# Kernel optimization log

Measured on AMD Instinct MI355X. Metric: run time of the kernel, lower is better.

The kernel has to match this reference:

```python
import jax, jax.numpy as jnp
import numpy as np

DIM = 384
HEADS = 6
HIDDEN = int(DIM * 4.0)
EPS = 1e-6

def setup_inputs() -> dict:
    key = jax.random.key(0)
    ks = jax.random.split(key, 8)
    s = 0.02
    return {
        "x": jax.random.normal(ks[0], (4, 2048, DIM), dtype=jnp.float32),
        "w_qkv": jax.random.normal(ks[1], (DIM, 3 * DIM), dtype=jnp.float32) * s,
        "b_qkv": jnp.zeros((3 * DIM,), dtype=jnp.float32),
        "w_proj": jax.random.normal(ks[2], (DIM, DIM), dtype=jnp.float32) * s,
        "b_proj": jnp.zeros((DIM,), dtype=jnp.float32),
        "w_fc1": jax.random.normal(ks[3], (DIM, HIDDEN), dtype=jnp.float32) * s,
        "b_fc1": jnp.zeros((HIDDEN,), dtype=jnp.float32),
        "w_fc2": jax.random.normal(ks[4], (HIDDEN, DIM), dtype=jnp.float32) * s,
        "b_fc2": jnp.zeros((DIM,), dtype=jnp.float32),
        "g1": jnp.ones((DIM,), dtype=jnp.float32),
        "beta1": jnp.zeros((DIM,), dtype=jnp.float32),
        "g2": jnp.ones((DIM,), dtype=jnp.float32),
        "beta2": jnp.zeros((DIM,), dtype=jnp.float32),
    }

def _layernorm(x, g, b):
    mu = jnp.mean(x, axis=-1, keepdims=True)
    var = jnp.mean(jnp.square(x - mu), axis=-1, keepdims=True)
    return (x - mu) * jax.lax.rsqrt(var + EPS) * g + b

def _attention(x, w_qkv, b_qkv, w_proj, b_proj):
    B, N, C = x.shape
    H = HEADS
    Dh = C // H
    qkv = x @ w_qkv + b_qkv                      # [B,N,3C]
    qkv = qkv.reshape(B, N, 3, H, Dh)
    q = jnp.transpose(qkv[:, :, 0], (0, 2, 1, 3))  # [B,H,N,Dh]
    k = jnp.transpose(qkv[:, :, 1], (0, 2, 1, 3))
    v = jnp.transpose(qkv[:, :, 2], (0, 2, 1, 3))
    scale = Dh ** -0.5
    attn = jnp.einsum('bhnd,bhmd->bhnm', q, k) * scale
    attn = jax.nn.softmax(attn, axis=-1)
    out = jnp.einsum('bhnm,bhmd->bhnd', attn, v)
    out = jnp.transpose(out, (0, 2, 1, 3)).reshape(B, N, C)
    return out @ w_proj + b_proj

def _mlp(x, w_fc1, b_fc1, w_fc2, b_fc2):
    h = jax.nn.gelu(x @ w_fc1 + b_fc1, approximate=False)
    return h @ w_fc2 + b_fc2

def reference(x, w_qkv, b_qkv, w_proj, b_proj, w_fc1, b_fc1, w_fc2, b_fc2, g1, beta1, g2, beta2):
    x = x + _attention(_layernorm(x, g1, beta1), w_qkv, b_qkv, w_proj, b_proj)
    x = x + _mlp(_layernorm(x, g2, beta2), w_fc1, b_fc1, w_fc2, b_fc2)
    return x
```

## Files before the change

### kernel.cpp

```cpp
#include <hip/hip_runtime.h>
#include <hip/hip_bf16.h>

#define TOK 8192
#define CDIM 384
#define HEADS 6
#define DH 64
#define HID 1536
#define SEQ 2048

#define QSCALE 0.18033688011112042f

typedef short bf16x8 __attribute__((ext_vector_type(8)));
typedef short bf16x4 __attribute__((ext_vector_type(4)));
typedef float f32x4 __attribute__((ext_vector_type(4)));
typedef float f32x16 __attribute__((ext_vector_type(16)));
typedef void __attribute__((address_space(1))) GV;
typedef void __attribute__((address_space(3))) SV;

__device__ __forceinline__ short f2bf(float f) {
    __hip_bfloat16 h = __float2bfloat16(f);
    return *reinterpret_cast<short*>(&h);
}

__device__ __forceinline__ int pack_bf2(float a, float b) {
    __hip_bfloat162 h2 = __float22bfloat162_rn(make_float2(a, b));
    int r;
    __builtin_memcpy(&r, &h2, 4);
    return r;
}

__device__ __forceinline__ void gl_lds16(const short* g, short* lds) {
    __builtin_amdgcn_global_load_lds((GV*)g, (SV*)lds, 16, 0, 0);
}

__device__ __forceinline__ float gelu_fast(float v) {
    const float A = 2.3022067f;
    const float B = 0.1029442f;
    const float u = v * (A + B * v * v);
    return v - v / (1.0f + exp2f(u));
}

__global__ __launch_bounds__(128) void ln_trans(const float* __restrict__ x,
                                                const float* __restrict__ g,
                                                const float* __restrict__ bta,
                                                short* __restrict__ y,
                                                const float* __restrict__ w_qkv,
                                                const float* __restrict__ w_proj,
                                                const float* __restrict__ w_fc1,
                                                const float* __restrict__ w_fc2,
                                                short* __restrict__ qkvT,
                                                short* __restrict__ projT,
                                                short* __restrict__ fc1T,
                                                short* __restrict__ fc2T) {
    if (blockIdx.x < TOK) {
        const int row = blockIdx.x;
        const float* xr = x + (size_t)row * CDIM;
        const int t = threadIdx.x;
        float v0 = xr[t], v1 = xr[t + 128], v2 = xr[t + 256];
        float s = v0 + v1 + v2;
        float ss = v0 * v0 + v1 * v1 + v2 * v2;
#pragma unroll
        for (int off = 1; off < 64; off <<= 1) {
            s += __shfl_xor(s, off);
            ss += __shfl_xor(ss, off);
        }
        __shared__ float sh[4];
        const int wv = t >> 6;
        if ((t & 63) == 0) { sh[wv] = s; sh[2 + wv] = ss; }
        __syncthreads();
        s = sh[0] + sh[1];
        ss = sh[2] + sh[3];
        const float mu = s * (1.0f / CDIM);
        const float var = ss * (1.0f / CDIM) - mu * mu;
        const float rs = rsqrtf(var + 1e-6f);
        short* yr = y + (size_t)row * CDIM;
        yr[t]       = f2bf((v0 - mu) * rs * g[t]       + bta[t]);
        yr[t + 128] = f2bf((v1 - mu) * rs * g[t + 128] + bta[t + 128]);
        yr[t + 256] = f2bf((v2 - mu) * rs * g[t + 256] + bta[t + 256]);
        return;
    }
    int b = blockIdx.x - TOK;
    const float* w; short* o; int K, N, nb;
    if (b < 432)       { w = w_qkv;  o = qkvT;  K = 384;  N = 1152; nb = 36; }
    else if (b < 576)  { b -= 432;  w = w_proj; o = projT; K = 384;  N = 384;  nb = 12; }
    else if (b < 1152) { b -= 576;  w = w_fc1;  o = fc1T;  K = 384;  N = 1536; nb = 48; }
    else               { b -= 1152; w = w_fc2;  o = fc2T;  K = 1536; N = 384;  nb = 12; }
    const int bx = (b % nb) * 32, by = (b / nb) * 32;
    __shared__ float t[32][33];
    const int tx = threadIdx.x & 31, ty = threadIdx.x >> 5;
#pragma unroll
    for (int i = 0; i < 8; ++i)
        t[ty + i * 4][tx] = w[(size_t)(by + ty + i * 4) * N + bx + tx];
    __syncthreads();
#pragma unroll
    for (int i = 0; i < 8; ++i)
        o[(size_t)(bx + ty + i * 4) * K + by + tx] = f2bf(t[tx][ty + i * 4]);
}

__global__ __launch_bounds__(128) void ln_kernel(const float* __restrict__ x,
                                                 const float* __restrict__ g,
                                                 const float* __restrict__ bta,
                                                 short* __restrict__ y) {
    const int row = blockIdx.x;
    const float* xr = x + (size_t)row * CDIM;
    const int t = threadIdx.x;
    float v0 = xr[t], v1 = xr[t + 128], v2 = xr[t + 256];
    float s = v0 + v1 + v2;
    float ss = v0 * v0 + v1 * v1 + v2 * v2;
#pragma unroll
    for (int off = 1; off < 64; off <<= 1) {
        s += __shfl_xor(s, off);
        ss += __shfl_xor(ss, off);
    }
    __shared__ float sh[4];
    const int wv = t >> 6;
    if ((t & 63) == 0) { sh[wv] = s; sh[2 + wv] = ss; }
    __syncthreads();
    s = sh[0] + sh[1];
    ss = sh[2] + sh[3];
    const float mu = s * (1.0f / CDIM);
    const float var = ss * (1.0f / CDIM) - mu * mu;
    const float rs = rsqrtf(var + 1e-6f);
    short* yr = y + (size_t)row * CDIM;
    yr[t]       = f2bf((v0 - mu) * rs * g[t]       + bta[t]);
    yr[t + 128] = f2bf((v1 - mu) * rs * g[t + 128] + bta[t + 128]);
    yr[t + 256] = f2bf((v2 - mu) * rs * g[t + 256] + bta[t + 256]);
}

template <int MODE, int MT>
__global__ __launch_bounds__(256) void mfma_gemm(const short* __restrict__ A,
                                                 const short* __restrict__ WT,
                                                 const float* __restrict__ bias,
                                                 const float* __restrict__ resid,
                                                 float* __restrict__ outF,
                                                 short* __restrict__ outB,
                                                 short* __restrict__ qb,
                                                 short* __restrict__ kb,
                                                 short* __restrict__ vtb,
                                                 int M, int N, int K) {
    constexpr int BN = (MT == 4) ? 128 : 64;
    constexpr int BM = (MT == 1) ? 64 : 128;
    __shared__ __align__(16) short As[BM * 64];
    __shared__ __align__(16) short Bs[BN * 64];

    const int tid  = threadIdx.x;
    const int w    = tid >> 6;
    const int lane = tid & 63;
    const int quad = lane >> 4;
    const int n15  = lane & 15;
    const int wr   = (MT == 4) ? (w >> 1) : w;
    const int wc   = (MT == 4) ? (w & 1) : 0;
    const int m0   = blockIdx.y * BM;
    const int n0   = blockIdx.x * BN;
    const int swz  = n15 & 7;

    f32x4 acc[MT][4];
#pragma unroll
    for (int i = 0; i < MT; ++i)
#pragma unroll
        for (int j = 0; j < 4; ++j) {
            acc[i][j][0] = 0; acc[i][j][1] = 0; acc[i][j][2] = 0; acc[i][j][3] = 0;
        }

    for (int k0 = 0; k0 < K; k0 += 64) {
        __syncthreads();
#pragma unroll
        for (int i = 0; i < BM / 32; ++i) {
            const int c = i * 256 + tid;
            const int r = c >> 3, p = c & 7;
            gl_lds16(A + (size_t)(m0 + r) * K + k0 + ((p ^ (r & 7)) * 8),
                     As + (i * 256 + w * 64) * 8);
        }
#pragma unroll
        for (int i = 0; i < BN / 32; ++i) {
            const int c = i * 256 + tid;
            const int r = c >> 3, p = c & 7;
            gl_lds16(WT + (size_t)(n0 + r) * K + k0 + ((p ^ (r & 7)) * 8),
                     Bs + (i * 256 + w * 64) * 8);
        }
        __syncthreads();

#pragma unroll
        for (int kk = 0; kk < 2; ++kk) {
            bf16x8 af[MT], bfr[4];
#pragma unroll
            for (int mt = 0; mt < MT; ++mt)
                af[mt] = *(const bf16x8*)&As[(wr * (MT * 16) + mt * 16 + n15) * 64 +
                                             (((kk * 4 + quad) ^ swz) * 8)];
#pragma unroll
            for (int nt = 0; nt < 4; ++nt)
                bfr[nt] = *(const bf16x8*)&Bs[(wc * 64 + nt * 16 + n15) * 64 +
                                              (((kk * 4 + quad) ^ swz) * 8)];
#pragma unroll
            for (int mt = 0; mt < MT; ++mt)
#pragma unroll
                for (int nt = 0; nt < 4; ++nt)
                    acc[mt][nt] = __builtin_amdgcn_mfma_f32_16x16x32_bf16(af[mt], bfr[nt], acc[mt][nt], 0, 0, 0);
        }
    }

#pragma unroll
    for (int nt = 0; nt < 4; ++nt) {
        const int col = n0 + wc * 64 + nt * 16 + n15;
        const float bv = bias[col];
        if constexpr (MODE == 2) {
            const int part = col / CDIM;
            const int rem  = col - part * CDIM;
            const int h    = rem >> 6;
            const int d    = rem & 63;
#pragma unroll
            for (int mt = 0; mt < MT; ++mt) {
                const int r0 = m0 + wr * (MT * 16) + mt * 16 + quad * 4;
                const int bi = r0 >> 11;
                const int n  = r0 & 2047;
                if (part == 2) {
                    short4 pkv;
                    pkv.x = f2bf(acc[mt][nt][0] + bv);
                    pkv.y = f2bf(acc[mt][nt][1] + bv);
                    pkv.z = f2bf(acc[mt][nt][2] + bv);
                    pkv.w = f2bf(acc[mt][nt][3] + bv);
                    *(short4*)&vtb[((size_t)(bi * HEADS + h) * DH + d) * SEQ + n] = pkv;
                } else {
                    short* dst = (part == 0 ? qb : kb) +
                                 ((size_t)(bi * HEADS + h) * SEQ + n) * DH + d;
#pragma unroll
                    for (int rr = 0; rr < 4; ++rr) {
                        float o = acc[mt][nt][rr] + bv;
                        if (part == 0) o *= QSCALE;
                        dst[(size_t)rr * DH] = f2bf(o);
                    }
                }
            }
        } else {
#pragma unroll
            for (int mt = 0; mt < MT; ++mt)
#pragma unroll
                for (int rr = 0; rr < 4; ++rr) {
                    const int r = m0 + wr * (MT * 16) + mt * 16 + quad * 4 + rr;
                    float o = acc[mt][nt][rr] + bv;
                    if constexpr (MODE == 1) {
                        outB[(size_t)r * N + col] = f2bf(gelu_fast(o));
                    } else {
                        if (resid) o += resid[(size_t)r * N + col];
                        outF[(size_t)r * N + col] = o;
                    }
                }
        }
    }
}

__global__ __launch_bounds__(256, 4) void attn_mfma(const short* __restrict__ qb,
                                                    const short* __restrict__ kb,
                                                    const short* __restrict__ vtb,
                                                    short* __restrict__ outp) {
    __shared__ __align__(16) char smem[33792];

    const int bid = blockIdx.x;
    const int x   = bid & 7;
    const int j   = bid >> 3;
    const int bh  = x * 3 + (j >> 6);
    const int qt  = j & 63;
    const int bi  = bh / HEADS;
    const int h   = bh - bi * HEADS;

    const int tid  = threadIdx.x;
    const int w    = tid >> 6;
    const int lane = tid & 63;
    const int l31  = lane & 31;
    const int hi   = lane >> 5;

    short* Kl  = (short*)(smem + w * 8192);
    short* Vtl = (short*)(smem + w * 8192 + 4096);

    const size_t headoff = (size_t)bh * SEQ * DH;

    bf16x8 qf[4];
    {
        const short* qg = qb + headoff + (size_t)(qt * 32 + l31) * DH + hi * 8;
#pragma unroll
        for (int kc = 0; kc < 4; ++kc)
            qf[kc] = *(const bf16x8*)(qg + kc * 16);
    }

    const int l3 = lane >> 3, l7 = lane & 7;
    const int l2 = lane >> 2, p4 = lane & 3;
    const short* kg = kb + headoff + (size_t)(w * 32 + l3) * DH + ((l7 ^ l3) * 8);
    const short* vg = vtb + (size_t)bh * DH * SEQ + (size_t)l2 * SEQ +
                      ((p4 ^ (l2 & 3)) * 8) + w * 32;

    const int swk = l31 & 7;
    const int swv = l31 & 3;
    const int krd = l31 * 64;
    const int vrd = l31 * 32;

    f32x16 O0 = {}, O1 = {};
    float lp = 0.0f;
    const f32x16 Zc = {};

    bf16x8 kreg[4], vreg[4];
#pragma unroll
    for (int i = 0; i < 4; ++i) {
        kreg[i] = *(const bf16x8*)(kg + i * 512);
        vreg[i] = *(const bf16x8*)(vg + (size_t)i * 16 * SEQ);
    }

#pragma unroll 2
    for (int t = 0; t < SEQ / 128; ++t) {
#pragma unroll
        for (int i = 0; i < 4; ++i) {
            *(bf16x8*)&Kl[i * 512 + lane * 8]  = kreg[i];
            *(bf16x8*)&Vtl[i * 512 + lane * 8] = vreg[i];
        }
        if (t < SEQ / 128 - 1) {
            const short* kgn = kg + (size_t)(t + 1) * 128 * DH;
            const short* vgn = vg + (t + 1) * 128;
#pragma unroll
            for (int i = 0; i < 4; ++i) {
                kreg[i] = *(const bf16x8*)(kgn + i * 512);
                vreg[i] = *(const bf16x8*)(vgn + (size_t)i * 16 * SEQ);
            }
        }
        asm volatile("s_waitcnt lgkmcnt(0)" ::: "memory");

        bf16x8 kf0 = *(const bf16x8*)&Kl[krd + (((0 + hi) ^ swk) * 8)];
        bf16x8 kf1 = *(const bf16x8*)&Kl[krd + (((2 + hi) ^ swk) * 8)];
        bf16x8 kf2 = *(const bf16x8*)&Kl[krd + (((4 + hi) ^ swk) * 8)];
        bf16x8 kf3 = *(const bf16x8*)&Kl[krd + (((6 + hi) ^ swk) * 8)];

        f32x16 S = __builtin_amdgcn_mfma_f32_32x32x16_bf16(kf0, qf[0], Zc, 0, 0, 0);
        S = __builtin_amdgcn_mfma_f32_32x32x16_bf16(kf1, qf[1], S, 0, 0, 0);
        S = __builtin_amdgcn_mfma_f32_32x32x16_bf16(kf2, qf[2], S, 0, 0, 0);
        S = __builtin_amdgcn_mfma_f32_32x32x16_bf16(kf3, qf[3], S, 0, 0, 0);

        bf16x8 v00 = *(const bf16x8*)&Vtl[vrd + ((hi ^ swv) * 8)];
        bf16x8 v01 = *(const bf16x8*)&Vtl[vrd + (((2 + hi) ^ swv) * 8)];
        bf16x8 v10 = *(const bf16x8*)&Vtl[1024 + vrd + ((hi ^ swv) * 8)];
        bf16x8 v11 = *(const bf16x8*)&Vtl[1024 + vrd + (((2 + hi) ^ swv) * 8)];

        float e[16];
#pragma unroll
        for (int r = 0; r < 16; ++r) e[r] = exp2f(S[r]);
        lp += (((e[0] + e[1]) + (e[2] + e[3])) + ((e[4] + e[5]) + (e[6] + e[7]))) +
              (((e[8] + e[9]) + (e[10] + e[11])) + ((e[12] + e[13]) + (e[14] + e[15])));

        int p0 = pack_bf2(e[0], e[1]),  p1 = pack_bf2(e[2], e[3]);
        int p2 = pack_bf2(e[4], e[5]),  p3 = pack_bf2(e[6], e[7]);
        asm("v_permlane32_swap_b32 %0, %1" : "+v"(p0), "+v"(p2));
        asm("v_permlane32_swap_b32 %0, %1" : "+v"(p1), "+v"(p3));
        int p4w = pack_bf2(e[8], e[9]),  p5 = pack_bf2(e[10], e[11]);
        int p6 = pack_bf2(e[12], e[13]), p7 = pack_bf2(e[14], e[15]);
        asm("v_permlane32_swap_b32 %0, %1" : "+v"(p4w), "+v"(p6));
        asm("v_permlane32_swap_b32 %0, %1" : "+v"(p5), "+v"(p7));
        bf16x8 pf0, pf1;
        { int pw[4] = {p0, p1, p2, p3};   __builtin_memcpy(&pf0, pw, 16); }
        { int pw[4] = {p4w, p5, p6, p7};  __builtin_memcpy(&pf1, pw, 16); }

        O0 = __builtin_amdgcn_mfma_f32_32x32x16_bf16(v00, pf0, O0, 0, 0, 0);
        O0 = __builtin_amdgcn_mfma_f32_32x32x16_bf16(v01, pf1, O0, 0, 0, 0);
        O1 = __builtin_amdgcn_mfma_f32_32x32x16_bf16(v10, pf0, O1, 0, 0, 0);
        O1 = __builtin_amdgcn_mfma_f32_32x32x16_bf16(v11, pf1, O1, 0, 0, 0);
    }

    lp += __shfl_xor(lp, 32);

    __syncthreads();
    float* Obuf = (float*)smem;
    float* lbuf = (float*)smem + 8320;
    float* myO  = Obuf + w * 2080;
#pragma unroll
    for (int r = 0; r < 16; ++r) {
        const int d0 = (r & 3) + 8 * (r >> 2) + 4 * hi;
        myO[l31 * 65 + d0]      = O0[r];
        myO[l31 * 65 + 32 + d0] = O1[r];
    }
    if (hi == 0) lbuf[w * 32 + l31] = lp;
    __syncthreads();

    const int quad = lane >> 4;
    const int n15  = lane & 15;
    const int d = w * 16 + n15;
#pragma unroll
    for (int i = 0; i < 8; ++i) {
        const int q = quad * 8 + i;
        const float l = lbuf[q] + lbuf[32 + q] + lbuf[64 + q] + lbuf[96 + q];
        const float s = Obuf[q * 65 + d] + Obuf[2080 + q * 65 + d] +
                        Obuf[4160 + q * 65 + d] + Obuf[6240 + q * 65 + d];
        outp[(size_t)(bi * SEQ + qt * 32 + q) * CDIM + h * DH + d] = f2bf(s / l);
    }
}

extern "C" void kernel_launch(void* const* d_in, const int* in_sizes, int n_in,
                              void* d_out, int out_size, void* d_ws, size_t ws_size,
                              hipStream_t stream) {
    const float* x      = (const float*)d_in[0];
    const float* w_qkv  = (const float*)d_in[1];
    const float* b_qkv  = (const float*)d_in[2];
    const float* w_proj = (const float*)d_in[3];
    const float* b_proj = (const float*)d_in[4];
    const float* w_fc1  = (const float*)d_in[5];
    const float* b_fc1  = (const float*)d_in[6];
    const float* w_fc2  = (const float*)d_in[7];
    const float* b_fc2  = (const float*)d_in[8];
    const float* g1     = (const float*)d_in[9];
    const float* beta1  = (const float*)d_in[10];
    const float* g2     = (const float*)d_in[11];
    const float* beta2  = (const float*)d_in[12];
    float* out = (float*)d_out;

    short* qkvT = (short*)d_ws;
    short* projT = qkvT + 1152 * 384;
    short* fc1T  = projT + 384 * 384;
    short* fc2T  = fc1T + 1536 * 384;
    short* y     = fc2T + 384 * 1536;
    short* qb    = y + (size_t)TOK * 384;
    short* kb    = qb + (size_t)TOK * 384;
    short* vtb   = kb + (size_t)TOK * 384;
    short* attn  = vtb + (size_t)TOK * 384;
    short* hbuf  = attn + (size_t)TOK * 384;

    ln_trans<<<TOK + 1728, 128, 0, stream>>>(x, g1, beta1, y,
                                             w_qkv, w_proj, w_fc1, w_fc2,
                                             qkvT, projT, fc1T, fc2T);
    mfma_gemm<2, 4><<<dim3(1152 / 128, TOK / 128), 256, 0, stream>>>(
        y, qkvT, b_qkv, nullptr, nullptr, nullptr, qb, kb, vtb, TOK, 3 * CDIM, CDIM);
    attn_mfma<<<1536, 256, 0, stream>>>(qb, kb, vtb, attn);
    mfma_gemm<0, 1><<<dim3(CDIM / 64, TOK / 64), 256, 0, stream>>>(
        attn, projT, b_proj, x, out, nullptr, nullptr, nullptr, nullptr, TOK, CDIM, CDIM);
    ln_kernel<<<TOK, 128, 0, stream>>>(out, g2, beta2, y);
    mfma_gemm<1, 4><<<dim3(HID / 128, TOK / 128), 256, 0, stream>>>(
        y, fc1T, b_fc1, nullptr, nullptr, hbuf, nullptr, nullptr, nullptr, TOK, HID, CDIM);
    mfma_gemm<0, 1><<<dim3(CDIM / 64, TOK / 64), 256, 0, stream>>>(
        hbuf, fc2T, b_fc2, out, out, nullptr, nullptr, nullptr, nullptr, TOK, CDIM, HID);
}
```

Measured before the change: 251.1 us.

## Use direct global-to-LDS double-buffered loads and halve attention waves per block

The attention kernel now runs 2 waves per block instead of 4, so each wave covers 1024 keys in 64-key steps instead of 512 keys in 128-key steps. K and V tiles move straight from global memory into LDS (gl_lds16) through a per-wave double buffer with vmcnt-based waits, replacing the register-staged copy. The final reduction of partial outputs and row sums now combines two waves instead of four. This aims to cut register pressure and VGPR-to-LDS store traffic and to overlap loads with compute. In exchange there are fewer waves per block and a longer serial loop per wave, and the launch bounds now allow fewer blocks per CU.

```diff
diff --git a/kernel.cpp b/kernel.cpp
--- a/kernel.cpp
+++ b/kernel.cpp
@@ -249,11 +249,11 @@
     }
 }
 
-__global__ __launch_bounds__(256, 4) void attn_mfma(const short* __restrict__ qb,
+__global__ __launch_bounds__(128, 2) void attn_mfma(const short* __restrict__ qb,
                                                     const short* __restrict__ kb,
                                                     const short* __restrict__ vtb,
                                                     short* __restrict__ outp) {
-    __shared__ __align__(16) char smem[33792];
+    __shared__ __align__(16) char smem[32768];
 
     const int bid = blockIdx.x;
     const int x   = bid & 7;
@@ -269,9 +269,6 @@
     const int l31  = lane & 31;
     const int hi   = lane >> 5;
 
-    short* Kl  = (short*)(smem + w * 8192);
-    short* Vtl = (short*)(smem + w * 8192 + 4096);
-
     const size_t headoff = (size_t)bh * SEQ * DH;
 
     bf16x8 qf[4];
@@ -281,6 +278,7 @@
         for (int kc = 0; kc < 4; ++kc)
             qf[kc] = *(const bf16x8*)(qg + kc * 16);
     }
+    asm volatile("s_waitcnt vmcnt(0)" ::: "memory");
 
     const int l3 = lane >> 3, l7 = lane & 7;
     const int l2 = lane >> 2, p4 = lane & 3;
@@ -297,45 +295,47 @@
     float lp = 0.0f;
     const f32x16 Zc = {};
 
-    bf16x8 kreg[4], vreg[4];
-#pragma unroll
-    for (int i = 0; i < 4; ++i) {
-        kreg[i] = *(const bf16x8*)(kg + i * 512);
-        vreg[i] = *(const bf16x8*)(vg + (size_t)i * 16 * SEQ);
-    }
+#define STAGE(tt)                                                                  \
+    {                                                                              \
+        short* Kd = (short*)(smem + w * 16384 + ((tt) & 1) * 8192);                \
+        const short* kgt = kg + (size_t)(tt) * 64 * DH;                            \
+        const short* vgt = vg + (tt) * 64;                                         \
+        _Pragma("unroll")                                                          \
+        for (int i = 0; i < 4; ++i) {                                              \
+            gl_lds16(kgt + i * 512, Kd + i * 512);                                 \
+            gl_lds16(vgt + (size_t)i * 16 * SEQ, Kd + 2048 + i * 512);             \
+        }                                                                          \
+    }
+
+    STAGE(0);
 
 #pragma unroll 2
-    for (int t = 0; t < SEQ / 128; ++t) {
-#pragma unroll
-        for (int i = 0; i < 4; ++i) {
-            *(bf16x8*)&Kl[i * 512 + lane * 8]  = kreg[i];
-            *(bf16x8*)&Vtl[i * 512 + lane * 8] = vreg[i];
-        }
-        if (t < SEQ / 128 - 1) {
-            const short* kgn = kg + (size_t)(t + 1) * 128 * DH;
-            const short* vgn = vg + (t + 1) * 128;
-#pragma unroll
-            for (int i = 0; i < 4; ++i) {
-                kreg[i] = *(const bf16x8*)(kgn + i * 512);
-                vreg[i] = *(const bf16x8*)(vgn + (size_t)i * 16 * SEQ);
-            }
-        }
-        asm volatile("s_waitcnt lgkmcnt(0)" ::: "memory");
-
-        bf16x8 kf0 = *(const bf16x8*)&Kl[krd + (((0 + hi) ^ swk) * 8)];
-        bf16x8 kf1 = *(const bf16x8*)&Kl[krd + (((2 + hi) ^ swk) * 8)];
-        bf16x8 kf2 = *(const bf16x8*)&Kl[krd + (((4 + hi) ^ swk) * 8)];
-        bf16x8 kf3 = *(const bf16x8*)&Kl[krd + (((6 + hi) ^ swk) * 8)];
+    for (int t = 0; t < SEQ / 64; ++t) {
+        if (t < SEQ / 64 - 1) {
+            STAGE(t + 1);
+            asm volatile("s_waitcnt vmcnt(8)" ::: "memory");
+        } else {
+            asm volatile("s_waitcnt vmcnt(0)" ::: "memory");
+        }
+        __builtin_amdgcn_wave_barrier();
+
+        const short* Klb  = (const short*)(smem + w * 16384 + (t & 1) * 8192);
+        const short* Vtlb = Klb + 2048;
+
+        bf16x8 kf0 = *(const bf16x8*)&Klb[krd + (((0 + hi) ^ swk) * 8)];
+        bf16x8 kf1 = *(const bf16x8*)&Klb[krd + (((2 + hi) ^ swk) * 8)];
+        bf16x8 kf2 = *(const bf16x8*)&Klb[krd + (((4 + hi) ^ swk) * 8)];
+        bf16x8 kf3 = *(const bf16x8*)&Klb[krd + (((6 + hi) ^ swk) * 8)];
 
         f32x16 S = __builtin_amdgcn_mfma_f32_32x32x16_bf16(kf0, qf[0], Zc, 0, 0, 0);
         S = __builtin_amdgcn_mfma_f32_32x32x16_bf16(kf1, qf[1], S, 0, 0, 0);
         S = __builtin_amdgcn_mfma_f32_32x32x16_bf16(kf2, qf[2], S, 0, 0, 0);
         S = __builtin_amdgcn_mfma_f32_32x32x16_bf16(kf3, qf[3], S, 0, 0, 0);
 
-        bf16x8 v00 = *(const bf16x8*)&Vtl[vrd + ((hi ^ swv) * 8)];
-        bf16x8 v01 = *(const bf16x8*)&Vtl[vrd + (((2 + hi) ^ swv) * 8)];
-        bf16x8 v10 = *(const bf16x8*)&Vtl[1024 + vrd + ((hi ^ swv) * 8)];
-        bf16x8 v11 = *(const bf16x8*)&Vtl[1024 + vrd + (((2 + hi) ^ swv) * 8)];
+        bf16x8 v00 = *(const bf16x8*)&Vtlb[vrd + ((hi ^ swv) * 8)];
+        bf16x8 v01 = *(const bf16x8*)&Vtlb[vrd + (((2 + hi) ^ swv) * 8)];
+        bf16x8 v10 = *(const bf16x8*)&Vtlb[1024 + vrd + ((hi ^ swv) * 8)];
+        bf16x8 v11 = *(const bf16x8*)&Vtlb[1024 + vrd + (((2 + hi) ^ swv) * 8)];
 
         float e[16];
 #pragma unroll
@@ -360,12 +360,13 @@
         O1 = __builtin_amdgcn_mfma_f32_32x32x16_bf16(v10, pf0, O1, 0, 0, 0);
         O1 = __builtin_amdgcn_mfma_f32_32x32x16_bf16(v11, pf1, O1, 0, 0, 0);
     }
+#undef STAGE
 
     lp += __shfl_xor(lp, 32);
 
     __syncthreads();
     float* Obuf = (float*)smem;
-    float* lbuf = (float*)smem + 8320;
+    float* lbuf = (float*)(smem + 16640);
     float* myO  = Obuf + w * 2080;
 #pragma unroll
     for (int r = 0; r < 16; ++r) {
@@ -376,15 +377,13 @@
     if (hi == 0) lbuf[w * 32 + l31] = lp;
     __syncthreads();
 
-    const int quad = lane >> 4;
-    const int n15  = lane & 15;
-    const int d = w * 16 + n15;
-#pragma unroll
-    for (int i = 0; i < 8; ++i) {
-        const int q = quad * 8 + i;
-        const float l = lbuf[q] + lbuf[32 + q] + lbuf[64 + q] + lbuf[96 + q];
-        const float s = Obuf[q * 65 + d] + Obuf[2080 + q * 65 + d] +
-                        Obuf[4160 + q * 65 + d] + Obuf[6240 + q * 65 + d];
+    const int d  = tid & 63;
+    const int qh = tid >> 6;
+#pragma unroll
+    for (int i = 0; i < 16; ++i) {
+        const int q = qh * 16 + i;
+        const float l = lbuf[q] + lbuf[32 + q];
+        const float s = Obuf[q * 65 + d] + Obuf[2080 + q * 65 + d];
         outp[(size_t)(bi * SEQ + qt * 32 + q) * CDIM + h * DH + d] = f2bf(s / l);
     }
 }
@@ -423,7 +422,7 @@
                                              qkvT, projT, fc1T, fc2T);
     mfma_gemm<2, 4><<<dim3(1152 / 128, TOK / 128), 256, 0, stream>>>(
         y, qkvT, b_qkv, nullptr, nullptr, nullptr, qb, kb, vtb, TOK, 3 * CDIM, CDIM);
-    attn_mfma<<<1536, 256, 0, stream>>>(qb, kb, vtb, attn);
+    attn_mfma<<<1536, 128, 0, stream>>>(qb, kb, vtb, attn);
     mfma_gemm<0, 1><<<dim3(CDIM / 64, TOK / 64), 256, 0, stream>>>(
         attn, projT, b_proj, x, out, nullptr, nullptr, nullptr, nullptr, TOK, CDIM, CDIM);
     ln_kernel<<<TOK, 128, 0, stream>>>(out, g2, beta2, y);
```

New measurement: 262.6 us. +4.6%, slower.
